# Performance work log

Hardware: AMD Instinct MI355X
Metric: run time of the kernel (lower is better)

## Reference

```python
import jax, jax.numpy as jnp
import numpy as np

N_TEX = 65536   # texture length N
C = 16          # channels
U = 4194304     # number of sample points


def setup_inputs() -> dict:
    key = jax.random.key(0)
    k1, k2 = jax.random.split(key)
    inp = jax.random.normal(k1, (N_TEX, C), dtype=jnp.float32)
    param = jax.random.uniform(k2, (U,), dtype=jnp.float32)  # normalized coords in [0,1]
    return {"input": inp, "param": param}


def reference(input, param):
    # 1D bilinear (linear) texture fetch: map param in [0,1] to [0, N-1]
    n = input.shape[0]
    t = param * (n - 1)                                   # (U,) continuous index
    i0 = jnp.clip(jnp.floor(t), 0, n - 1).astype(jnp.int32)
    i1 = jnp.clip(i0 + 1, 0, n - 1)
    w = (t - i0.astype(t.dtype))[:, None]                 # (U,1) interp weight
    # gather + interpolate -> (U, C)
    return input[i0] * (1.0 - w) + input[i1] * w
```

## Files before the change

### kernel.cpp

```cpp
#include <hip/hip_runtime.h>

#define N_TEX 65536
#define C 16
#define U 4194304
#define ILP 4

typedef float    f32x4 __attribute__((ext_vector_type(4)));
typedef int      i32x4 __attribute__((ext_vector_type(4)));
typedef _Float16 f16x4 __attribute__((ext_vector_type(4)));

__global__ __launch_bounds__(256) void convert_kernel(
    const f32x4* __restrict__ in, f16x4* __restrict__ out16)
{
    const int i = blockIdx.x * 256 + threadIdx.x;
    f32x4 v = __builtin_nontemporal_load(&in[i]);
    f16x4 h;
    h.x = (_Float16)v.x; h.y = (_Float16)v.y;
    h.z = (_Float16)v.z; h.w = (_Float16)v.w;
    out16[i] = h;
}

__global__ __launch_bounds__(256) void warm_kernel(
    const i32x4* __restrict__ texv, const f32x4* __restrict__ paramv)
{
    const int b = blockIdx.x;
    const int t = threadIdx.x;

    const int i = t >> 5;
    const int g = t & 31;
    const int s = (b & 7) + 8 * ((b >> 3) * 8 + i);
    const int k0 = g >> 4;
    const int m  = g & 15;
    f32x4 p0 = paramv[s * 16 + m + k0 * 262144];
    f32x4 p1 = paramv[s * 16 + m + (k0 + 2) * 262144];

    const int cbase = (b >> 3) * 512 + t * 2;
    i32x4 t0 = texv[cbase];
    i32x4 t1 = texv[cbase + 1];

    asm volatile("" :: "v"(p0), "v"(p1), "v"(t0), "v"(t1));
}

__global__ __launch_bounds__(256) void sampler1d_kernel(
    const f16x4* __restrict__ tex16, const float* __restrict__ param,
    f32x4* __restrict__ out)
{
    const int NT  = (U * 4) / ILP;
    const int tid = blockIdx.x * 256 + threadIdx.x;
    const int q   = tid & 3;

    float p[ILP];
#pragma unroll
    for (int k = 0; k < ILP; ++k)
        p[k] = __builtin_nontemporal_load(&param[(tid + k * NT) >> 2]);

    float w[ILP];
    f16x4 a[ILP], b[ILP];
#pragma unroll
    for (int k = 0; k < ILP; ++k) {
        const float t = p[k] * (float)(N_TEX - 1);
        float f = floorf(t);
        f = fminf(fmaxf(f, 0.0f), (float)(N_TEX - 1));
        const int i0 = (int)f;
        const int i1 = min(i0 + 1, N_TEX - 1);
        w[k] = t - f;
        a[k] = tex16[i0 * 4 + q];
        b[k] = tex16[i1 * 4 + q];
    }

#pragma unroll
    for (int k = 0; k < ILP; ++k) {
        const float wk = w[k], iw = 1.0f - wk;
        f32x4 r;
        r.x = (float)a[k].x * iw + (float)b[k].x * wk;
        r.y = (float)a[k].y * iw + (float)b[k].y * wk;
        r.z = (float)a[k].z * iw + (float)b[k].z * wk;
        r.w = (float)a[k].w * iw + (float)b[k].w * wk;
        __builtin_nontemporal_store(r, &out[tid + k * NT]);
    }
}

extern "C" void kernel_launch(void* const* d_in, const int* in_sizes, int n_in,
                              void* d_out, int out_size, void* d_ws, size_t ws_size,
                              hipStream_t stream) {
    const f32x4* tex32 = (const f32x4*)d_in[0];
    const float* param = (const float*)d_in[1];
    f32x4*       out   = (f32x4*)d_out;
    f16x4*       tex16 = (f16x4*)d_ws;

    const int total_thr = (U * 4) / ILP;

    convert_kernel<<<(N_TEX * C / 4) / 256, 256, 0, stream>>>(tex32, tex16);
    warm_kernel<<<2048, 256, 0, stream>>>((const i32x4*)tex16, (const f32x4*)param);
    sampler1d_kernel<<<total_thr / 256, 256, 0, stream>>>(tex16, param, out);
}
```

Measured before the change: 85.68 us.

## Interleave neighbor texels into fp16 pair table for single-gather interpolation

Replaces the fp16 texture copy with a pair table in which each entry interleaves texel i and texel i+1 per channel. The sampler then needs one 16-byte gather per sample instead of two 8-byte gathers, which halves the number of gather instructions. The cost is that the table doubles to 4 MB, and the warm kernel is reworked to prefetch the larger table into cache with three spread reads per block. The bigger footprint may put more pressure on L2/MALL, and the build kernel reads each input row twice.

```diff
diff --git a/kernel.cpp b/kernel.cpp
--- a/kernel.cpp
+++ b/kernel.cpp
@@ -7,42 +7,54 @@
 
 typedef float    f32x4 __attribute__((ext_vector_type(4)));
 typedef int      i32x4 __attribute__((ext_vector_type(4)));
-typedef _Float16 f16x4 __attribute__((ext_vector_type(4)));
+typedef _Float16 f16x8 __attribute__((ext_vector_type(8)));
 
-__global__ __launch_bounds__(256) void convert_kernel(
-    const f32x4* __restrict__ in, f16x4* __restrict__ out16)
+__global__ __launch_bounds__(256) void build_pairs_kernel(
+    const f32x4* __restrict__ in, f16x8* __restrict__ pairs)
 {
-    const int i = blockIdx.x * 256 + threadIdx.x;
-    f32x4 v = __builtin_nontemporal_load(&in[i]);
-    f16x4 h;
-    h.x = (_Float16)v.x; h.y = (_Float16)v.y;
-    h.z = (_Float16)v.z; h.w = (_Float16)v.w;
-    out16[i] = h;
+    const int id = blockIdx.x * 256 + threadIdx.x;
+    const int i  = id >> 2;
+    const int q  = id & 3;
+    const int ip = min(i + 1, N_TEX - 1);
+    const f32x4 a = in[i * 4 + q];
+    const f32x4 b = in[ip * 4 + q];
+    f16x8 o;
+    o[0] = (_Float16)a.x; o[1] = (_Float16)b.x;
+    o[2] = (_Float16)a.y; o[3] = (_Float16)b.y;
+    o[4] = (_Float16)a.z; o[5] = (_Float16)b.z;
+    o[6] = (_Float16)a.w; o[7] = (_Float16)b.w;
+    pairs[id] = o;
 }
 
 __global__ __launch_bounds__(256) void warm_kernel(
-    const i32x4* __restrict__ texv, const f32x4* __restrict__ paramv)
+    const i32x4* __restrict__ tabv, const f32x4* __restrict__ paramv)
 {
     const int b = blockIdx.x;
     const int t = threadIdx.x;
 
-    const int i = t >> 5;
-    const int g = t & 31;
-    const int s = (b & 7) + 8 * ((b >> 3) * 8 + i);
+    const int i  = t >> 5;
+    const int g  = t & 31;
+    const int s  = (b & 7) + 8 * ((b >> 3) * 8 + i);
     const int k0 = g >> 4;
     const int m  = g & 15;
     f32x4 p0 = paramv[s * 16 + m + k0 * 262144];
     f32x4 p1 = paramv[s * 16 + m + (k0 + 2) * 262144];
+    asm volatile("" :: "v"(p0), "v"(p1));
 
-    const int cbase = (b >> 3) * 512 + t * 2;
-    i32x4 t0 = texv[cbase];
-    i32x4 t1 = texv[cbase + 1];
-
-    asm volatile("" :: "v"(p0), "v"(p1), "v"(t0), "v"(t1));
+#pragma unroll
+    for (int r = 0; r < 3; ++r) {
+        const int c    = ((b >> 3) + r * 85) & 255;
+        const int base = c * 1024 + t * 4;
+        i32x4 t0 = tabv[base + 0];
+        i32x4 t1 = tabv[base + 1];
+        i32x4 t2 = tabv[base + 2];
+        i32x4 t3 = tabv[base + 3];
+        asm volatile("" :: "v"(t0), "v"(t1), "v"(t2), "v"(t3));
+    }
 }
 
 __global__ __launch_bounds__(256) void sampler1d_kernel(
-    const f16x4* __restrict__ tex16, const float* __restrict__ param,
+    const f16x8* __restrict__ pairs, const float* __restrict__ param,
     f32x4* __restrict__ out)
 {
     const int NT  = (U * 4) / ILP;
@@ -55,27 +67,23 @@
         p[k] = __builtin_nontemporal_load(&param[(tid + k * NT) >> 2]);
 
     float w[ILP];
-    f16x4 a[ILP], b[ILP];
+    f16x8 v[ILP];
 #pragma unroll
     for (int k = 0; k < ILP; ++k) {
         const float t = p[k] * (float)(N_TEX - 1);
-        float f = floorf(t);
-        f = fminf(fmaxf(f, 0.0f), (float)(N_TEX - 1));
-        const int i0 = (int)f;
-        const int i1 = min(i0 + 1, N_TEX - 1);
+        float f = fminf(fmaxf(floorf(t), 0.0f), (float)(N_TEX - 1));
         w[k] = t - f;
-        a[k] = tex16[i0 * 4 + q];
-        b[k] = tex16[i1 * 4 + q];
+        v[k] = pairs[(int)f * 4 + q];
     }
 
 #pragma unroll
     for (int k = 0; k < ILP; ++k) {
         const float wk = w[k], iw = 1.0f - wk;
         f32x4 r;
-        r.x = (float)a[k].x * iw + (float)b[k].x * wk;
-        r.y = (float)a[k].y * iw + (float)b[k].y * wk;
-        r.z = (float)a[k].z * iw + (float)b[k].z * wk;
-        r.w = (float)a[k].w * iw + (float)b[k].w * wk;
+        r.x = (float)v[k][0] * iw + (float)v[k][1] * wk;
+        r.y = (float)v[k][2] * iw + (float)v[k][3] * wk;
+        r.z = (float)v[k][4] * iw + (float)v[k][5] * wk;
+        r.w = (float)v[k][6] * iw + (float)v[k][7] * wk;
         __builtin_nontemporal_store(r, &out[tid + k * NT]);
     }
 }
@@ -86,11 +94,11 @@
     const f32x4* tex32 = (const f32x4*)d_in[0];
     const float* param = (const float*)d_in[1];
     f32x4*       out   = (f32x4*)d_out;
-    f16x4*       tex16 = (f16x4*)d_ws;
+    f16x8*       pairs = (f16x8*)d_ws;
 
     const int total_thr = (U * 4) / ILP;
 
-    convert_kernel<<<(N_TEX * C / 4) / 256, 256, 0, stream>>>(tex32, tex16);
-    warm_kernel<<<2048, 256, 0, stream>>>((const i32x4*)tex16, (const f32x4*)param);
-    sampler1d_kernel<<<total_thr / 256, 256, 0, stream>>>(tex16, param, out);
+    build_pairs_kernel<<<(N_TEX * 4) / 256, 256, 0, stream>>>(tex32, pairs);
+    warm_kernel<<<2048, 256, 0, stream>>>((const i32x4*)pairs, (const f32x4*)param);
+    sampler1d_kernel<<<total_thr / 256, 256, 0, stream>>>(pairs, param, out);
 }
```

Result: slower. 100.8 us (+17.7%).

## Convert sampler to persistent grid with double-buffered software-pipelined gathers

Applied to the files above, without the earlier changes.

The sampler kernel drops from one 16-unit pass per thread over 16384 blocks to a fixed grid of 2048 blocks. Each thread loops over batches, prefetching params two batches ahead and issuing texture gathers one batch ahead, while it interpolates and stores the current batch. The goal is to overlap gather latency with stores inside each wave instead of depending on wave-level occupancy. The cost is more live registers and fewer waves in flight, and the sched_barrier limits how far the compiler can reorder instructions.

```diff
diff --git a/kernel.cpp b/kernel.cpp
--- a/kernel.cpp
+++ b/kernel.cpp
@@ -3,7 +3,12 @@
 #define N_TEX 65536
 #define C 16
 #define U 4194304
-#define ILP 4
+#define TPB 256
+#define NBLK 2048
+#define NTHREADS (NBLK * TPB)
+#define UNITS (U * 4)
+#define BATCH 4
+#define NBATCH (UNITS / NTHREADS / BATCH)
 
 typedef float    f32x4 __attribute__((ext_vector_type(4)));
 typedef int      i32x4 __attribute__((ext_vector_type(4)));
@@ -25,7 +30,6 @@
 {
     const int b = blockIdx.x;
     const int t = threadIdx.x;
-
     const int i = t >> 5;
     const int g = t & 31;
     const int s = (b & 7) + 8 * ((b >> 3) * 8 + i);
@@ -33,11 +37,9 @@
     const int m  = g & 15;
     f32x4 p0 = paramv[s * 16 + m + k0 * 262144];
     f32x4 p1 = paramv[s * 16 + m + (k0 + 2) * 262144];
-
     const int cbase = (b >> 3) * 512 + t * 2;
     i32x4 t0 = texv[cbase];
     i32x4 t1 = texv[cbase + 1];
-
     asm volatile("" :: "v"(p0), "v"(p1), "v"(t0), "v"(t1));
 }
 
@@ -45,38 +47,63 @@
     const f16x4* __restrict__ tex16, const float* __restrict__ param,
     f32x4* __restrict__ out)
 {
-    const int NT  = (U * 4) / ILP;
-    const int tid = blockIdx.x * 256 + threadIdx.x;
+    const int tid = blockIdx.x * TPB + threadIdx.x;
     const int q   = tid & 3;
 
-    float p[ILP];
+    float p[2][BATCH];
+    float w[2][BATCH];
+    f16x4 ga[2][BATCH], gb[2][BATCH];
+
 #pragma unroll
-    for (int k = 0; k < ILP; ++k)
-        p[k] = __builtin_nontemporal_load(&param[(tid + k * NT) >> 2]);
-
-    float w[ILP];
-    f16x4 a[ILP], b[ILP];
+    for (int k = 0; k < BATCH; ++k)
+        p[0][k] = __builtin_nontemporal_load(&param[(tid + k * NTHREADS) >> 2]);
 #pragma unroll
-    for (int k = 0; k < ILP; ++k) {
-        const float t = p[k] * (float)(N_TEX - 1);
-        float f = floorf(t);
-        f = fminf(fmaxf(f, 0.0f), (float)(N_TEX - 1));
+    for (int k = 0; k < BATCH; ++k)
+        p[1][k] = __builtin_nontemporal_load(&param[(tid + (BATCH + k) * NTHREADS) >> 2]);
+#pragma unroll
+    for (int k = 0; k < BATCH; ++k) {
+        const float t = p[0][k] * (float)(N_TEX - 1);
+        const float f = fminf(fmaxf(floorf(t), 0.0f), (float)(N_TEX - 1));
         const int i0 = (int)f;
         const int i1 = min(i0 + 1, N_TEX - 1);
-        w[k] = t - f;
-        a[k] = tex16[i0 * 4 + q];
-        b[k] = tex16[i1 * 4 + q];
+        w[0][k]  = t - f;
+        ga[0][k] = tex16[i0 * 4 + q];
+        gb[0][k] = tex16[i1 * 4 + q];
     }
 
 #pragma unroll
-    for (int k = 0; k < ILP; ++k) {
-        const float wk = w[k], iw = 1.0f - wk;
-        f32x4 r;
-        r.x = (float)a[k].x * iw + (float)b[k].x * wk;
-        r.y = (float)a[k].y * iw + (float)b[k].y * wk;
-        r.z = (float)a[k].z * iw + (float)b[k].z * wk;
-        r.w = (float)a[k].w * iw + (float)b[k].w * wk;
-        __builtin_nontemporal_store(r, &out[tid + k * NT]);
+    for (int j = 0; j < NBATCH; ++j) {
+        const int cur = j & 1, nxt = (j + 1) & 1;
+
+        if (j + 1 < NBATCH) {
+#pragma unroll
+            for (int k = 0; k < BATCH; ++k) {
+                const float t = p[nxt][k] * (float)(N_TEX - 1);
+                const float f = fminf(fmaxf(floorf(t), 0.0f), (float)(N_TEX - 1));
+                const int i0 = (int)f;
+                const int i1 = min(i0 + 1, N_TEX - 1);
+                w[nxt][k]  = t - f;
+                ga[nxt][k] = tex16[i0 * 4 + q];
+                gb[nxt][k] = tex16[i1 * 4 + q];
+            }
+        }
+        if (j + 2 < NBATCH) {
+#pragma unroll
+            for (int k = 0; k < BATCH; ++k)
+                p[cur][k] = __builtin_nontemporal_load(
+                    &param[(tid + ((j + 2) * BATCH + k) * NTHREADS) >> 2]);
+        }
+#pragma unroll
+        for (int k = 0; k < BATCH; ++k) {
+            const float wk = w[cur][k], iw = 1.0f - wk;
+            f32x4 r;
+            r.x = (float)ga[cur][k].x * iw + (float)gb[cur][k].x * wk;
+            r.y = (float)ga[cur][k].y * iw + (float)gb[cur][k].y * wk;
+            r.z = (float)ga[cur][k].z * iw + (float)gb[cur][k].z * wk;
+            r.w = (float)ga[cur][k].w * iw + (float)gb[cur][k].w * wk;
+            __builtin_nontemporal_store(r, &out[tid + (j * BATCH + k) * NTHREADS]);
+        }
+        __builtin_amdgcn_sched_barrier(0);
     }
 }
 
@@ -88,9 +115,7 @@
     f32x4*       out   = (f32x4*)d_out;
     f16x4*       tex16 = (f16x4*)d_ws;
 
-    const int total_thr = (U * 4) / ILP;
-
     convert_kernel<<<(N_TEX * C / 4) / 256, 256, 0, stream>>>(tex32, tex16);
     warm_kernel<<<2048, 256, 0, stream>>>((const i32x4*)tex16, (const f32x4*)param);
-    sampler1d_kernel<<<total_thr / 256, 256, 0, stream>>>(tex16, param, out);
+    sampler1d_kernel<<<NBLK, TPB, 0, stream>>>(tex16, param, out);
 }
```

Result: slower. 93.22 us (+8.8%).
